# Kernel tuning notes

Hardware: AMD Instinct MI355X
Metric: run time of the kernel (lower is better)

The kernel has to match this reference:

```python
import jax, jax.numpy as jnp
import numpy as np

POOLED = 7          # square pooled grid (grid_width == grid_height required by torch_combined_meshgrid)
NUM_LEVELS = 6      # len_feature_maps; level = clamp(floor(5 + log2(sqrt(w*h))), 0, 5)


def _bilinear_sample(fm, gx, gy):
    """fm: [C, D, D]; gx, gy: [N, G, G] normalized coords in [0,1].
    Faithful to getWeightedSum_ofFourFmapPoints: floor/ceil corner points with
    proportion weights; coord dim 0 (x) indexes fmap rows, dim 1 (y) indexes cols.
    Returns [N, C, G, G]."""
    D = fm.shape[-1]
    ux = gx * (D - 1)
    uy = gy * (D - 1)
    x0 = jnp.floor(ux); x1 = jnp.ceil(ux)
    y0 = jnp.floor(uy); y1 = jnp.ceil(uy)
    ddx = jnp.where(x1 - x0 == 0, 1.0, x1 - x0)
    ddy = jnp.where(y1 - y0 == 0, 1.0, y1 - y0)
    px0 = 1.0 - (ux - x0) / ddx   # proportion_to_take_from_start_x
    px1 = 1.0 - px0
    py0 = 1.0 - (uy - y0) / ddy
    py1 = 1.0 - py0
    ix0 = x0.astype(jnp.int32); ix1 = x1.astype(jnp.int32)
    iy0 = y0.astype(jnp.int32); iy1 = y1.astype(jnp.int32)
    # advanced indexing: fm[:, idx, idx] -> [C, N, G, G]
    tl = fm[:, ix0, iy0]
    tr = fm[:, ix1, iy0]
    bl = fm[:, ix0, iy1]
    br = fm[:, ix1, iy1]
    w_tl = (px0 * py0)[None]
    w_tr = (px1 * py0)[None]
    w_bl = (px0 * py1)[None]
    w_br = (px1 * py1)[None]
    pooled = w_tl * tl + w_tr * tr + w_bl * bl + w_br * br  # [C, N, G, G]
    return jnp.moveaxis(pooled, 0, 1)                        # [N, C, G, G]


def setup_inputs() -> dict:
    key = jax.random.key(0)
    N, C = 2000, 256
    dims = [38, 19, 10, 5, 3, 1]
    kw, kh, kx, ky, *kf = jax.random.split(key, 4 + len(dims))
    w = jax.random.uniform(kw, (N, 1), minval=0.02, maxval=0.98)
    h = jax.random.uniform(kh, (N, 1), minval=0.02, maxval=0.98)
    x1 = jax.random.uniform(kx, (N, 1)) * (1.0 - w)
    y1 = jax.random.uniform(ky, (N, 1)) * (1.0 - h)
    boxes = jnp.concatenate([x1, y1, x1 + w, y1 + h], axis=1)  # x1 y1 x2 y2 in [0,1]
    out = {"boxes": boxes}
    for i, (d, k) in enumerate(zip(dims, kf)):
        out[f"fmap{i}"] = jax.random.normal(k, (1, C, d, d), dtype=jnp.float32)
    return out


def reference(boxes, fmap0, fmap1, fmap2, fmap3, fmap4, fmap5):
    fmaps = [fmap0, fmap1, fmap2, fmap3, fmap4, fmap5]
    N = boxes.shape[0]
    C = fmap0.shape[1]
    G = POOLED
    x1, y1, x2, y2 = boxes[:, 0:1], boxes[:, 1:2], boxes[:, 2:3], boxes[:, 3:4]
    # FPN-style level index: floor(5 + log2(sqrt(w*h))), clamped (constant w.r.t. grad)
    avg = jnp.sqrt((x2 - x1) * (y2 - y1))
    lvl = jnp.clip(jnp.floor((NUM_LEVELS - 1.0) + jnp.log2(avg)), 0, NUM_LEVELS - 1)
    lvl = jax.lax.stop_gradient(lvl.astype(jnp.int32).reshape(-1))  # [N]
    # bilinear interpolation grid: grid[n,i,j] = (x1 + i*dx/(G-1), y1 + j*dy/(G-1)), clamped
    t = jnp.arange(G, dtype=boxes.dtype)
    denom = max(1.0, G - 1.0)
    xr = jnp.clip(x1 + t[None, :] * (x2 - x1) / denom, 0.0, 1.0)  # [N, G]
    yr = jnp.clip(y1 + t[None, :] * (y2 - y1) / denom, 0.0, 1.0)  # [N, G]
    gx = jnp.broadcast_to(xr[:, :, None], (N, G, G))
    gy = jnp.broadcast_to(yr[:, None, :], (N, G, G))
    out = jnp.zeros((N, C, G, G), dtype=fmap0.dtype)
    for l, f in enumerate(fmaps):
        fm = f[0]  # [C, D, D] (single image; one fmap selected per box)
        if fm.shape[-1] == 1:
            # original returns fmap[:, :, 0:1, 0:1]; broadcast the constant to the grid
            pooled = jnp.broadcast_to(fm[None, :, :1, :1], (N, C, G, G))
        else:
            pooled = _bilinear_sample(fm, gx, gy)
        mask = (lvl == l).astype(fmap0.dtype)[:, None, None, None]
        out = out + mask * pooled
    return out
```

## Files before the change

kernel.cpp:

```cpp
#include <hip/hip_runtime.h>

#define G 7
#define CCH 256
#define NLVL 6

__device__ __constant__ int kD[NLVL]  = {38, 19, 10, 5, 3, 1};
__device__ __constant__ int kD2[NLVL] = {1444, 361, 100, 25, 9, 1};
__device__ __constant__ int kBaseT[NLVL + 1] = {0, 369664, 462080, 487680, 494080, 496384, 496640};

#define FMT_TOTAL 496640

__global__ __launch_bounds__(256) void transpose_fmaps(
    const float* __restrict__ f0, const float* __restrict__ f1,
    const float* __restrict__ f2, const float* __restrict__ f3,
    const float* __restrict__ f4, const float* __restrict__ f5,
    float* __restrict__ fmT)
{
    int o = blockIdx.x * blockDim.x + threadIdx.x;
    if (o >= FMT_TOTAL) return;
    int l = 0;
#pragma unroll
    for (int k = 1; k < NLVL; ++k) l += (o >= kBaseT[k]);
    int rel = o - kBaseT[l];
    int p = rel >> 8;
    int c = rel & 255;
    const float* f;
    switch (l) {
        case 0: f = f0; break;
        case 1: f = f1; break;
        case 2: f = f2; break;
        case 3: f = f3; break;
        case 4: f = f4; break;
        default: f = f5; break;
    }
    fmT[o] = f[c * kD2[l] + p];
}

__global__ __launch_bounds__(256) void roialign_main(
    const float* __restrict__ boxes, const float* __restrict__ fmT,
    float* __restrict__ out)
{
    __shared__ float sOut[CCH * 49];
    __shared__ float4 sW[49];
    __shared__ int4 sOff[49];

    int n = blockIdx.x;
    int tid = threadIdx.x;

    if (tid < 49) {
        float bx1 = boxes[n * 4 + 0];
        float by1 = boxes[n * 4 + 1];
        float bx2 = boxes[n * 4 + 2];
        float by2 = boxes[n * 4 + 3];
        float w = bx2 - bx1;
        float h = by2 - by1;
        float avg = sqrtf(w * h);
        float lf = floorf((float)(NLVL - 1) + log2f(avg));
        lf = fminf(fmaxf(lf, 0.0f), (float)(NLVL - 1));
        int lvl = (int)lf;
        int D = kD[lvl];
        float Dm1 = (float)(D - 1);
        int base = kBaseT[lvl];

        int i = tid / 7;
        int j = tid - i * 7;
        float xr = fminf(fmaxf(bx1 + ((float)i * w) / 6.0f, 0.0f), 1.0f);
        float yr = fminf(fmaxf(by1 + ((float)j * h) / 6.0f, 0.0f), 1.0f);
        float ux = xr * Dm1;
        float uy = yr * Dm1;
        float x0 = floorf(ux);
        float y0 = floorf(uy);
        int ix0 = (int)x0;
        int iy0 = (int)y0;
        float fx = ux - x0;
        float fy = uy - y0;
        int ix1 = min(ix0 + 1, D - 1);
        int iy1 = min(iy0 + 1, D - 1);

        sOff[tid] = make_int4(base + (ix0 * D + iy0) * CCH,
                              base + (ix1 * D + iy0) * CCH,
                              base + (ix0 * D + iy1) * CCH,
                              base + (ix1 * D + iy1) * CCH);
        float px0 = 1.0f - fx, py0 = 1.0f - fy;
        sW[tid] = make_float4(px0 * py0, fx * py0, px0 * fy, fx * fy);
    }
    __syncthreads();

#pragma unroll 7
    for (int g = 0; g < 49; ++g) {
        int4 o = sOff[g];
        float4 wv = sW[g];
        float v = wv.x * fmT[o.x + tid] + wv.y * fmT[o.y + tid]
                + wv.z * fmT[o.z + tid] + wv.w * fmT[o.w + tid];
        sOut[tid * 49 + g] = v;
    }

    asm volatile("s_waitcnt lgkmcnt(0)" ::: "memory");
    __builtin_amdgcn_sched_barrier(0);

    int wv_id = tid >> 6;
    int lane = tid & 63;
    const float4* s4 = (const float4*)sOut + wv_id * 784;
    float4* out4 = (float4*)(out + (size_t)n * (CCH * G * G)) + wv_id * 784;
#pragma unroll
    for (int k = 0; k < 12; ++k) {
        out4[k * 64 + lane] = s4[k * 64 + lane];
    }
    if (lane < 16) out4[768 + lane] = s4[768 + lane];
}

__global__ __launch_bounds__(256) void roialign_fallback(
    const float* __restrict__ boxes,
    const float* __restrict__ f0, const float* __restrict__ f1,
    const float* __restrict__ f2, const float* __restrict__ f3,
    const float* __restrict__ f4, const float* __restrict__ f5,
    float* __restrict__ out, int total4)
{
    int t = blockIdx.x * blockDim.x + threadIdx.x;
    if (t >= total4) return;
    const int perN = CCH * G * G;
    int idx = t * 4;
    int n = idx / perN;
    int rem = idx - n * perN;
    float bx1 = boxes[n * 4 + 0], by1 = boxes[n * 4 + 1];
    float bx2 = boxes[n * 4 + 2], by2 = boxes[n * 4 + 3];
    float w = bx2 - bx1, h = by2 - by1;
    float avg = sqrtf(w * h);
    float lf = floorf((float)(NLVL - 1) + log2f(avg));
    lf = fminf(fmaxf(lf, 0.0f), (float)(NLVL - 1));
    int lvl = (int)lf;
    const float* fm;
    switch (lvl) {
        case 0: fm = f0; break;
        case 1: fm = f1; break;
        case 2: fm = f2; break;
        case 3: fm = f3; break;
        case 4: fm = f4; break;
        default: fm = f5; break;
    }
    int D = kD[lvl];
    float Dm1 = (float)(D - 1);
    float4 res;
    float* rp = &res.x;
#pragma unroll
    for (int k = 0; k < 4; ++k) {
        int e = rem + k;
        int j = e % G;
        int iq = e / G;
        int i = iq % G;
        int c = iq / G;
        float xr = fminf(fmaxf(bx1 + ((float)i * w) / 6.0f, 0.0f), 1.0f);
        float yr = fminf(fmaxf(by1 + ((float)j * h) / 6.0f, 0.0f), 1.0f);
        float ux = xr * Dm1, uy = yr * Dm1;
        float x0 = floorf(ux), y0 = floorf(uy);
        int ix0 = (int)x0, iy0 = (int)y0;
        float fx = ux - x0, fy = uy - y0;
        int ix1 = min(ix0 + 1, D - 1), iy1 = min(iy0 + 1, D - 1);
        const float* p = fm + c * D * D;
        float v00 = p[ix0 * D + iy0], v10 = p[ix1 * D + iy0];
        float v01 = p[ix0 * D + iy1], v11 = p[ix1 * D + iy1];
        float px0 = 1.0f - fx, py0 = 1.0f - fy;
        rp[k] = px0 * py0 * v00 + fx * py0 * v10 + px0 * fy * v01 + fx * fy * v11;
    }
    reinterpret_cast<float4*>(out)[t] = res;
}

extern "C" void kernel_launch(void* const* d_in, const int* in_sizes, int n_in,
                              void* d_out, int out_size, void* d_ws, size_t ws_size,
                              hipStream_t stream) {
    const float* boxes = (const float*)d_in[0];
    const float* f0 = (const float*)d_in[1];
    const float* f1 = (const float*)d_in[2];
    const float* f2 = (const float*)d_in[3];
    const float* f3 = (const float*)d_in[4];
    const float* f4 = (const float*)d_in[5];
    const float* f5 = (const float*)d_in[6];
    float* out = (float*)d_out;
    int N = in_sizes[0] / 4;

    if (ws_size >= (size_t)FMT_TOTAL * sizeof(float)) {
        float* fmT = (float*)d_ws;
        transpose_fmaps<<<(FMT_TOTAL + 255) / 256, 256, 0, stream>>>(
            f0, f1, f2, f3, f4, f5, fmT);
        roialign_main<<<N, 256, 0, stream>>>(boxes, fmT, out);
    } else {
        int total4 = out_size / 4;
        roialign_fallback<<<(total4 + 255) / 256, 256, 0, stream>>>(
            boxes, f0, f1, f2, f3, f4, f5, out, total4);
    }
}
```

Before: 34.71 us.

## Separate bilinear interpolation into x then y passes to reduce gathers

Adds a separable path: for each of the 7 x rows it interpolates along x at only the distinct y columns covered (NY, at most 7), staging the partial results in shared memory, then interpolates along y into 49 register accumulators. This is meant to cut global gathers from 196 to at most 98 per channel. The original 4-corner path is kept for boxes whose y span needs more than 7 columns. The cost is extra LDS traffic, a 49-float register array that may raise register pressure, and a variable inner loop trip count.

```diff
diff --git a/kernel.cpp b/kernel.cpp
--- a/kernel.cpp
+++ b/kernel.cpp
@@ -40,9 +40,15 @@
     const float* __restrict__ boxes, const float* __restrict__ fmT,
     float* __restrict__ out)
 {
-    __shared__ float sOut[CCH * 49];
+    __shared__ float  sOut[CCH * 49];
+    __shared__ int4   sOff[49];
     __shared__ float4 sW[49];
-    __shared__ int4 sOff[49];
+    __shared__ float  sXw[7][2];
+    __shared__ int    sXo[7][2];
+    __shared__ float  sYw[7][2];
+    __shared__ int    sYv[7][2];
+    __shared__ int    sYoff[7];
+    __shared__ int    sMeta[2];
 
     int n = blockIdx.x;
     int tid = threadIdx.x;
@@ -83,16 +89,78 @@
                               base + (ix1 * D + iy1) * CCH);
         float px0 = 1.0f - fx, py0 = 1.0f - fy;
         sW[tid] = make_float4(px0 * py0, fx * py0, px0 * fy, fx * fy);
+
+        if (tid < 7) {
+            int ii = tid;
+            float xr2 = fminf(fmaxf(bx1 + ((float)ii * w) / 6.0f, 0.0f), 1.0f);
+            float ux2 = xr2 * Dm1;
+            float x02 = floorf(ux2);
+            int jx0 = (int)x02;
+            float fx2 = ux2 - x02;
+            int jx1 = min(jx0 + 1, D - 1);
+            sXw[ii][0] = 1.0f - fx2;
+            sXw[ii][1] = fx2;
+            sXo[ii][0] = base + jx0 * D * CCH;
+            sXo[ii][1] = base + jx1 * D * CCH;
+            float yr2 = fminf(fmaxf(by1 + ((float)ii * h) / 6.0f, 0.0f), 1.0f);
+            float uy2 = yr2 * Dm1;
+            float y02 = floorf(uy2);
+            int jy0 = (int)y02;
+            float fy2 = uy2 - y02;
+            int jy1 = min(jy0 + 1, D - 1);
+            sYw[ii][0] = 1.0f - fy2;
+            sYw[ii][1] = fy2;
+            int y00 = __shfl(jy0, 0);
+            int y06 = __shfl(jy0, 6);
+            int NY = y06 - y00 + 2;
+            sYv[ii][0] = jy0 - y00;
+            sYv[ii][1] = jy1 - y00;
+            sYoff[ii] = min(y00 + ii, D - 1) * CCH;
+            if (ii == 0) { sMeta[0] = NY; sMeta[1] = (NY > 7) ? 1 : 0; }
+        }
     }
     __syncthreads();
 
+    int rowb = tid * 49;
+
+    if (!sMeta[1]) {
+        int NY = sMeta[0];
+#pragma unroll
+        for (int i = 0; i < 7; ++i) {
+            float px0 = sXw[i][0], px1 = sXw[i][1];
+            int oA = sXo[i][0] + tid;
+            int oB = sXo[i][1] + tid;
+            int hb = rowb + i * NY;
+            for (int v = 0; v < NY; ++v) {
+                int oy = sYoff[v];
+                float A = fmT[oA + oy];
+                float B = fmT[oB + oy];
+                sOut[hb + v] = px0 * A + px1 * B;
+            }
+        }
+        float acc[49];
+#pragma unroll
+        for (int j = 0; j < 7; ++j) {
+            float py0 = sYw[j][0], py1 = sYw[j][1];
+            int vLo = sYv[j][0], vHi = sYv[j][1];
+#pragma unroll
+            for (int i = 0; i < 7; ++i) {
+                float hLo = sOut[rowb + i * NY + vLo];
+                float hHi = sOut[rowb + i * NY + vHi];
+                acc[i * 7 + j] = py0 * hLo + py1 * hHi;
+            }
+        }
+#pragma unroll
+        for (int g = 0; g < 49; ++g) sOut[rowb + g] = acc[g];
+    } else {
 #pragma unroll 7
-    for (int g = 0; g < 49; ++g) {
-        int4 o = sOff[g];
-        float4 wv = sW[g];
-        float v = wv.x * fmT[o.x + tid] + wv.y * fmT[o.y + tid]
-                + wv.z * fmT[o.z + tid] + wv.w * fmT[o.w + tid];
-        sOut[tid * 49 + g] = v;
+        for (int g = 0; g < 49; ++g) {
+            int4 o = sOff[g];
+            float4 w4 = sW[g];
+            float v = w4.x * fmT[o.x + tid] + w4.y * fmT[o.y + tid]
+                    + w4.z * fmT[o.z + tid] + w4.w * fmT[o.w + tid];
+            sOut[rowb + g] = v;
+        }
     }
 
     asm volatile("s_waitcnt lgkmcnt(0)" ::: "memory");
```

Measured after the change: 37.78 us. 8.8% more time.
